# Kernel tuning notes

Hardware: AMD Instinct MI355X
Metric: run time of the kernel (lower is better)

Reference implementation:

```python
import jax, jax.numpy as jnp
import numpy as np
from jax import lax

EPS_LN = 1e-5
EPS_NORM = 1e-12
NUM_HEADS = 8
KV_HEADS = 2
REP = NUM_HEADS // KV_HEADS


def _layernorm_c(x, w, b):
    # WithBias LayerNorm over channel dim; x: [b,c,h,w]
    mu = x.mean(axis=1, keepdims=True)
    var = ((x - mu) ** 2).mean(axis=1, keepdims=True)
    return (x - mu) / jnp.sqrt(var + EPS_LN) * w[None, :, None, None] + b[None, :, None, None]


def _conv1x1(x, w):
    # x: [b,c,h,w], w: [o,c]
    return jnp.einsum('bchw,oc->bohw', x, w)


def _dwconv3x3(x, w):
    # depthwise 3x3, SAME padding; w: [C,1,3,3]
    C = x.shape[1]
    return lax.conv_general_dilated(
        x, w, window_strides=(1, 1), padding='SAME',
        dimension_numbers=('NCHW', 'OIHW', 'NCHW'), feature_group_count=C)


def _l2norm(x):
    # normalize over last axis (torch F.normalize semantics)
    n = jnp.sqrt(jnp.sum(x * x, axis=-1, keepdims=True))
    return x / jnp.maximum(n, EPS_NORM)


def setup_inputs() -> dict:
    key = jax.random.key(0)
    ks = jax.random.split(key, 8)
    b, dim, h, w = 4, 192, 256, 256
    kv_ch = 2 * dim // REP  # 96
    return {
        'x': jax.random.normal(ks[0], (b, dim, h, w), jnp.float32),
        'ln_w': jnp.ones((dim,), jnp.float32),
        'ln_b': jnp.zeros((dim,), jnp.float32),
        'q_w': jax.random.normal(ks[1], (dim, dim), jnp.float32) * 0.02,
        'q_dw': jax.random.normal(ks[2], (dim, 1, 3, 3), jnp.float32) * 0.1,
        'kv_w': jax.random.normal(ks[3], (kv_ch, dim), jnp.float32) * 0.02,
        'kv_dw': jax.random.normal(ks[4], (kv_ch, 1, 3, 3), jnp.float32) * 0.1,
        'proj_w': jax.random.normal(ks[5], (dim, dim), jnp.float32) * 0.02,
        'temperature': jnp.ones((NUM_HEADS, 1, 1), jnp.float32),
    }


def reference(x, ln_w, ln_b, q_w, q_dw, kv_w, kv_dw, proj_w, temperature):
    b, c, h, w = x.shape
    xn = _layernorm_c(x, ln_w, ln_b)
    q = _dwconv3x3(_conv1x1(xn, q_w), q_dw)            # [b, c, h, w]
    kv = _dwconv3x3(_conv1x1(xn, kv_w), kv_dw)         # [b, 2c/rep, h, w]
    k, v = jnp.split(kv, 2, axis=1)
    hw = h * w
    ch = c // NUM_HEADS
    q = q.reshape(b, NUM_HEADS, ch, hw)
    k = k.reshape(b, KV_HEADS, ch, hw)
    v = v.reshape(b, KV_HEADS, ch, hw)
    k = jnp.repeat(k, REP, axis=1)                     # repeat_kv
    v = jnp.repeat(v, REP, axis=1)
    q = _l2norm(q)
    k = _l2norm(k)
    attn = jnp.einsum('bhcn,bhdn->bhcd', q, k) * temperature[None]
    attn = jax.nn.softmax(attn, axis=-1)
    out = jnp.einsum('bhcd,bhdn->bhcn', attn, v)
    out = out.reshape(b, c, h, w)
    return _conv1x1(out, proj_w)
```

## Files before the change

### kernel.cpp

```cpp
#include <hip/hip_runtime.h>
#include <hip/hip_bf16.h>
#include <stdint.h>

#define HW    65536
#define NB    4
#define CIN   192
#define OYC   288
#define BSTR  200
#define EPS2  264

__device__ __forceinline__ float bflo(unsigned u){ return __uint_as_float(u << 16); }
__device__ __forceinline__ float bfhi(unsigned u){ return __uint_as_float(u & 0xffff0000u); }
__device__ __forceinline__ float bf2f(__hip_bfloat16 v){ return __bfloat162float(v); }
__device__ __forceinline__ unsigned short f2bfbits(float f){
  __hip_bfloat16 h = __float2bfloat16(f); return *(unsigned short*)&h;
}

__device__ __forceinline__ void unpack8(uint4 u, float* f) {
  f[0]=bflo(u.x); f[1]=bfhi(u.x); f[2]=bflo(u.y); f[3]=bfhi(u.y);
  f[4]=bflo(u.z); f[5]=bfhi(u.z); f[6]=bflo(u.w); f[7]=bfhi(u.w);
}

union BF8 { uint4 u; __hip_bfloat16 h[8]; };

typedef __attribute__((ext_vector_type(8))) short short8;
typedef __attribute__((ext_vector_type(4))) float floatx4;

__global__ void k_prep(const float* __restrict__ qw, const float* __restrict__ kvw,
                       const float* __restrict__ lnw, const float* __restrict__ lnb,
                       __hip_bfloat16* __restrict__ AF, float* __restrict__ bias,
                       float* __restrict__ Ssum) {
  int blk = blockIdx.x, t = threadIdx.x;
  if (blk < 32) {
    for (int i = blk * 256 + t; i < OYC * CIN; i += 32 * 256) {
      int o = i / CIN, c = i % CIN;
      float w = (o < 192) ? qw[o * 192 + c] : kvw[(o - 192) * 192 + c];
      float val = w * lnw[c];
      int ot = o >> 4, lo = o & 15;
      int ks = c >> 5, cr = c & 31, q = cr >> 3, j = cr & 7;
      int dst = (((ot * 6 + ks) * 64) + q * 16 + lo) * 8 + j;
      AF[dst] = __float2bfloat16(val);
    }
  } else {
    for (int o = t; o < OYC; o += 256) {
      float s = 0.f, s2 = 0.f;
      for (int c = 0; c < CIN; ++c) {
        float w = (o < 192) ? qw[o * 192 + c] : kvw[(o - 192) * 192 + c];
        s += w * lnb[c];
        s2 += bf2f(__float2bfloat16(w * lnw[c]));
      }
      bias[o] = s;
      Ssum[o] = s2;
    }
  }
}

__global__ __launch_bounds__(512, 2) void k_conv1r(const float* __restrict__ x,
                                                   const __hip_bfloat16* __restrict__ AF,
                                                   const float* __restrict__ bias,
                                                   const float* __restrict__ Ssum,
                                                   __hip_bfloat16* __restrict__ y) {
  __shared__ __align__(16) __hip_bfloat16 Bl[256 * BSTR];
  __shared__ float part_s[8][256];
  __shared__ float part_q[8][256];
  __shared__ float murs[256][2];
  __shared__ float biasl[OYC];
  __shared__ float Sl[OYC];

  int bid = blockIdx.x;
  int b = bid >> 8;
  int r = bid & 255;
  int tid = threadIdx.x;
  int w = tid >> 6, l = tid & 63;

  for (int i = tid; i < OYC; i += 512) { biasl[i] = bias[i]; Sl[i] = Ssum[i]; }

  {
    const float* xb = x + (size_t)(b * CIN + w * 24) * HW + r * 256 + l * 4;
    float s[4] = {0.f, 0.f, 0.f, 0.f}, q2[4] = {0.f, 0.f, 0.f, 0.f};
    unsigned pk[4][12];
#pragma unroll
    for (int c = 0; c < 24; ++c) {
      float4 v4 = *(const float4*)(xb + (size_t)c * HW);
      float vv[4] = {v4.x, v4.y, v4.z, v4.w};
#pragma unroll
      for (int i = 0; i < 4; ++i) {
        s[i] += vv[i]; q2[i] += vv[i] * vv[i];
        unsigned bits = f2bfbits(vv[i]);
        if ((c & 1) == 0) pk[i][c >> 1] = bits;
        else              pk[i][c >> 1] |= bits << 16;
      }
    }
#pragma unroll
    for (int i = 0; i < 4; ++i) {
      int px = l * 4 + i;
#pragma unroll
      for (int j = 0; j < 3; ++j) {
        uint4 u = make_uint4(pk[i][j*4], pk[i][j*4+1], pk[i][j*4+2], pk[i][j*4+3]);
        *(uint4*)&Bl[px * BSTR + w * 24 + j * 8] = u;
      }
    }
    *(float4*)&part_s[w][l * 4] = make_float4(s[0], s[1], s[2], s[3]);
    *(float4*)&part_q[w][l * 4] = make_float4(q2[0], q2[1], q2[2], q2[3]);
  }
  __syncthreads();

  int lane = tid & 63;
  int mh = w >> 2, nq = w & 3;
  int li = lane & 15, qd = lane >> 4;

  floatx4 acc[9][4];
#pragma unroll
  for (int t = 0; t < 9; ++t)
#pragma unroll
    for (int nt = 0; nt < 4; ++nt) acc[t][nt] = (floatx4){0.f, 0.f, 0.f, 0.f};

  const __hip_bfloat16* abase = AF + ((size_t)(mh * 9) * 6 * 64 + lane) * 8;
  short8 a0[9], a1[9];
#pragma unroll
  for (int t = 0; t < 9; ++t) a0[t] = *(const short8*)(abase + (size_t)(t * 6) * 512);

#pragma unroll
  for (int ks = 0; ks < 6; ++ks) {
    short8 bf[4];
#pragma unroll
    for (int nt = 0; nt < 4; ++nt) {
      int px = nq * 64 + nt * 16 + li;
      bf[nt] = *(const short8*)&Bl[px * BSTR + ks * 32 + qd * 8];
    }
    if (ks < 5) {
#pragma unroll
      for (int t = 0; t < 9; ++t) {
        short8 v = *(const short8*)(abase + (size_t)(t * 6 + ks + 1) * 512);
        if (ks & 1) a0[t] = v; else a1[t] = v;
      }
    }
#pragma unroll
    for (int t = 0; t < 9; ++t) {
      short8 af = (ks & 1) ? a1[t] : a0[t];
#pragma unroll
      for (int nt = 0; nt < 4; ++nt)
        acc[t][nt] = __builtin_amdgcn_mfma_f32_16x16x32_bf16(af, bf[nt], acc[t][nt], 0, 0, 0);
    }
  }

  if (tid < 256) {
    float s0 = 0.f, s1 = 0.f;
#pragma unroll
    for (int g = 0; g < 8; ++g) { s0 += part_s[g][tid]; s1 += part_q[g][tid]; }
    float m = s0 * (1.f / CIN);
    float var = s1 * (1.f / CIN) - m * m;
    murs[tid][0] = m;
    murs[tid][1] = rsqrtf(var + 1e-5f);
  }

  __hip_bfloat16* EP = Bl;
#pragma unroll
  for (int ph = 0; ph < 2; ++ph) {
    __syncthreads();
    if (mh == ph) {
#pragma unroll
      for (int t = 0; t < 9; ++t)
#pragma unroll
        for (int nt = 0; nt < 4; ++nt) {
          int px = nq * 64 + nt * 16 + li;
          float mu = murs[px][0], rs = murs[px][1];
#pragma unroll
          for (int rr = 0; rr < 4; ++rr) {
            int ol = t * 16 + qd * 4 + rr;
            float val = rs * (acc[t][nt][rr] - mu * Sl[ph * 144 + ol]) + biasl[ph * 144 + ol];
            EP[ol * EPS2 + px] = __float2bfloat16(val);
          }
        }
    }
    __syncthreads();
    for (int i = tid; i < 144 * 32; i += 512) {
      int row = i >> 5, seg = i & 31;
      uint4 u = *(const uint4*)&EP[row * EPS2 + seg * 8];
      *(uint4*)&y[(size_t)(b * OYC + ph * 144 + row) * HW + r * 256 + seg * 8] = u;
    }
  }
}

__global__ __launch_bounds__(256) void k_dwkv(const __hip_bfloat16* __restrict__ y,
                                              const float* __restrict__ kvdw,
                                              __hip_bfloat16* __restrict__ kbuf,
                                              __hip_bfloat16* __restrict__ vbuf,
                                              float* __restrict__ kss) {
  __shared__ __align__(16) __hip_bfloat16 stage[18 * 256];
  int bid = blockIdx.x;
  int hb = bid & 15;
  int ck = (bid >> 4) % 96;
  int b  = bid / (16 * 96);
  int tid = threadIdx.x;
  int h0 = hb * 16;

  const __hip_bfloat16* yp = y + (size_t)(b * OYC + 192 + ck) * HW;
  for (int i = tid; i < 18 * 32; i += 256) {
    int ry = i >> 5, seg = i & 31;
    int hh = h0 - 1 + ry;
    uint4 u = make_uint4(0u, 0u, 0u, 0u);
    if ((unsigned)hh < 256u) u = *(const uint4*)(yp + hh * 256 + seg * 8);
    *(uint4*)&stage[ry * 256 + seg * 8] = u;
  }
  __syncthreads();

  float w[9];
#pragma unroll
  for (int i = 0; i < 9; ++i) w[i] = kvdw[ck * 9 + i];

  int cg = tid & 31, rg = tid >> 5;
  int c0 = cg * 8;
  bool isk = (ck < 48);
  __hip_bfloat16* ob = (isk ? kbuf : vbuf) + (size_t)(b * 48 + (ck % 48)) * HW;
  float ssq = 0.f;
#pragma unroll
  for (int rr = 0; rr < 2; ++rr) {
    int orow = rg * 2 + rr;
    float o[8];
#pragma unroll
    for (int j = 0; j < 8; ++j) o[j] = 0.f;
#pragma unroll
    for (int ry = 0; ry < 3; ++ry) {
      const __hip_bfloat16* rb = &stage[(orow + ry) * 256];
      float v[8];
      unpack8(*(const uint4*)&rb[c0], v);
      float vl = (c0 > 0)       ? bf2f(rb[c0 - 1]) : 0.f;
      float vr = (c0 + 8 < 256) ? bf2f(rb[c0 + 8]) : 0.f;
      float wl = w[ry * 3], wm = w[ry * 3 + 1], wr = w[ry * 3 + 2];
      o[0] = fmaf(wl, vl, fmaf(wm, v[0], fmaf(wr, v[1], o[0])));
#pragma unroll
      for (int j = 1; j < 7; ++j)
        o[j] = fmaf(wl, v[j-1], fmaf(wm, v[j], fmaf(wr, v[j+1], o[j])));
      o[7] = fmaf(wl, v[6], fmaf(wm, v[7], fmaf(wr, vr, o[7])));
    }
    BF8 t;
#pragma unroll
    for (int j = 0; j < 8; ++j) {
      t.h[j] = __float2bfloat16(o[j]);
      if (isk) { float fv = bf2f(t.h[j]); ssq += fv * fv; }
    }
    *(uint4*)(ob + (size_t)(h0 + orow) * 256 + c0) = t.u;
  }
  if (isk) {
#pragma unroll
    for (int off = 32; off > 0; off >>= 1) ssq += __shfl_down(ssq, off);
    __shared__ float ws4[4];
    if ((tid & 63) == 0) ws4[tid >> 6] = ssq;
    __syncthreads();
    if (tid == 0) atomicAdd(&kss[b * 48 + ck], ws4[0] + ws4[1] + ws4[2] + ws4[3]);
  }
}

__global__ __launch_bounds__(512) void k_dwqk(const __hip_bfloat16* __restrict__ y,
                                              const float* __restrict__ qdw,
                                              const __hip_bfloat16* __restrict__ kbuf,
                                              float* __restrict__ qss,
                                              float* __restrict__ attn) {
  __shared__ __align__(16) __hip_bfloat16 ys[32 * 6 * 256];
  __shared__ __align__(16) __hip_bfloat16 ql[32 * 264];
  __shared__ __align__(16) __hip_bfloat16 kl[24 * 264];
  __shared__ float red[32 * 33];
  __shared__ float qssl[32];

  int t = blockIdx.x;
  int band = t & 63; t >>= 6;
  int qh = t % 3; t /= 3;
  int kvh = t & 1;
  int b = t >> 1;
  int tid = threadIdx.x;
  int r0 = band * 4;
  int chg0 = kvh * 96 + qh * 32;

  for (int i = tid; i < 32 * 33; i += 512) red[i] = 0.f;
  if (tid < 32) qssl[tid] = 0.f;

  for (int i = tid; i < 6144; i += 512) {
    int ch = i / 192, rem = i % 192;
    int ry = rem >> 5, seg = rem & 31;
    int hh = r0 - 1 + ry;
    uint4 u = make_uint4(0u, 0u, 0u, 0u);
    if ((unsigned)hh < 256u)
      u = *(const uint4*)(y + (size_t)(b * OYC + chg0 + ch) * HW + hh * 256 + seg * 8);
    *(uint4*)&ys[(ch * 6 + ry) * 256 + seg * 8] = u;
  }
  __syncthreads();

  int wv = tid >> 6, lane = tid & 63;
  int li = lane & 15, qd = lane >> 4;
  int kr1 = 16 + li; if (kr1 > 23) kr1 = 23;

  floatx4 acc[2][2];
  acc[0][0] = (floatx4){0.f,0.f,0.f,0.f}; acc[0][1] = (floatx4){0.f,0.f,0.f,0.f};
  acc[1][0] = (floatx4){0.f,0.f,0.f,0.f}; acc[1][1] = (floatx4){0.f,0.f,0.f,0.f};

  const __hip_bfloat16* kp = kbuf + (size_t)(b * 48 + kvh * 24) * HW;

  for (int rr = 0; rr < 4; ++rr) {
    if (rr) __syncthreads();
    for (int i = tid; i < 1024; i += 512) {
      int ch = i >> 5, seg = i & 31, c0 = seg * 8;
      const float* wp = qdw + (chg0 + ch) * 9;
      float o[8];
#pragma unroll
      for (int j = 0; j < 8; ++j) o[j] = 0.f;
#pragma unroll
      for (int ry = 0; ry < 3; ++ry) {
        const __hip_bfloat16* rb = &ys[(ch * 6 + rr + ry) * 256];
        float v[8];
        unpack8(*(const uint4*)&rb[c0], v);
        float vl = (c0 > 0)       ? bf2f(rb[c0 - 1]) : 0.f;
        float vr = (c0 + 8 < 256) ? bf2f(rb[c0 + 8]) : 0.f;
        float wl = wp[ry * 3], wm = wp[ry * 3 + 1], wr = wp[ry * 3 + 2];
        o[0] = fmaf(wl, vl, fmaf(wm, v[0], fmaf(wr, v[1], o[0])));
#pragma unroll
        for (int j = 1; j < 7; ++j)
          o[j] = fmaf(wl, v[j-1], fmaf(wm, v[j], fmaf(wr, v[j+1], o[j])));
        o[7] = fmaf(wl, v[6], fmaf(wm, v[7], fmaf(wr, vr, o[7])));
      }
      BF8 u; float part = 0.f;
#pragma unroll
      for (int j = 0; j < 8; ++j) {
        u.h[j] = __float2bfloat16(o[j]);
        float fv = bf2f(u.h[j]); part += fv * fv;
      }
      *(uint4*)&ql[ch * 264 + c0] = u.u;
      atomicAdd(&qssl[ch], part);
    }
    for (int i = tid; i < 768; i += 512) {
      int ch = i >> 5, seg = i & 31;
      *(uint4*)&kl[ch * 264 + seg * 8] =
        *(const uint4*)(kp + (size_t)ch * HW + (r0 + rr) * 256 + seg * 8);
    }
    __syncthreads();
    {
      int off = wv * 32 + qd * 8;
      short8 bk0 = *(const short8*)&kl[li  * 264 + off];
      short8 bk1 = *(const short8*)&kl[kr1 * 264 + off];
#pragma unroll
      for (int mt = 0; mt < 2; ++mt) {
        short8 aq = *(const short8*)&ql[(mt * 16 + li) * 264 + off];
        acc[mt][0] = __builtin_amdgcn_mfma_f32_16x16x32_bf16(aq, bk0, acc[mt][0], 0, 0, 0);
        acc[mt][1] = __builtin_amdgcn_mfma_f32_16x16x32_bf16(aq, bk1, acc[mt][1], 0, 0, 0);
      }
    }
  }
  __syncthreads();
#pragma unroll
  for (int mt = 0; mt < 2; ++mt) {
#pragma unroll
    for (int nt = 0; nt < 2; ++nt) {
      int n = nt * 16 + li;
      if (n < 24) {
#pragma unroll
        for (int r = 0; r < 4; ++r) {
          int m = mt * 16 + qd * 4 + r;
          atomicAdd(&red[m * 33 + n], acc[mt][nt][r]);
        }
      }
    }
  }
  __syncthreads();
  for (int i = tid; i < 32 * 24; i += 512) {
    int m = i / 24, d = i % 24;
    int cc = qh * 32 + m;
    int head = kvh * 4 + cc / 24, cp = cc % 24;
    atomicAdd(&attn[(((b * 8 + head) * 24) + cp) * 24 + d], red[m * 33 + d]);
  }
  if (tid < 32) atomicAdd(&qss[b * 192 + chg0 + tid], qssl[tid]);
}

__global__ void k_attn_final(const float* __restrict__ attn, const float* __restrict__ qss,
                             const float* __restrict__ kss, const float* __restrict__ temp,
                             const float* __restrict__ projw, __hip_bfloat16* __restrict__ AB) {
  int b = blockIdx.x;
  int t = threadIdx.x;
  __shared__ float as_[96 * 25];
  float acc[48];
#pragma unroll
  for (int j = 0; j < 48; ++j) acc[j] = 0.f;
  for (int kvh = 0; kvh < 2; ++kvh) {
    __syncthreads();
    if (t < 96) {
      int row = kvh * 96 + t;
      int h = row / 24, cp = row % 24;
      float rq = 1.f / fmaxf(sqrtf(qss[b * 192 + row]), 1e-12f);
      float tp = temp[h];
      float lg[24]; float mx = -1e30f;
#pragma unroll
      for (int d = 0; d < 24; ++d) {
        float rk = 1.f / fmaxf(sqrtf(kss[b * 48 + kvh * 24 + d]), 1e-12f);
        float l = attn[(((b * 8 + h) * 24) + cp) * 24 + d] * rq * rk * tp;
        lg[d] = l; mx = fmaxf(mx, l);
      }
      float s = 0.f;
#pragma unroll
      for (int d = 0; d < 24; ++d) { lg[d] = __expf(lg[d] - mx); s += lg[d]; }
      float inv = 1.f / s;
#pragma unroll
      for (int d = 0; d < 24; ++d) as_[t * 25 + d] = lg[d] * inv;
    }
    __syncthreads();
    if (t < 192) {
      for (int cc = 0; cc < 96; ++cc) {
        float pw = projw[t * 192 + kvh * 96 + cc];
        const float* ar = &as_[cc * 25];
#pragma unroll
        for (int d = 0; d < 24; ++d) acc[kvh * 24 + d] = fmaf(pw, ar[d], acc[kvh * 24 + d]);
      }
    }
  }
  if (t < 192) {
    __hip_bfloat16* ABb = AB + (size_t)b * 18432;
    int mt = t >> 4, lb = t & 15;
#pragma unroll
    for (int g = 0; g < 12; ++g) {
      int kk0 = g * 8;
      int s = kk0 >> 5;
      int lane = lb + 16 * ((kk0 & 31) >> 3);
      BF8 u;
#pragma unroll
      for (int jj = 0; jj < 8; ++jj) {
        int kk = kk0 + jj;
        if (kk < 48) {
          u.h[jj] = __float2bfloat16(acc[kk]);
        } else {
          int j = kk - 48;
          float hv = bf2f(__float2bfloat16(acc[j]));
          u.h[jj] = __float2bfloat16(acc[j] - hv);
        }
      }
      *(uint4*)(ABb + (size_t)((mt * 3 + s) * 64 + lane) * 8) = u.u;
    }
  }
}

__global__ __launch_bounds__(512) void k_out(const __hip_bfloat16* __restrict__ vbuf,
                                             const __hip_bfloat16* __restrict__ AB,
                                             float* __restrict__ out) {
  __shared__ __align__(16) __hip_bfloat16 vT[256 * 56];
  __shared__ __align__(16) float EPu[48 * 260];
  __hip_bfloat16* vl = (__hip_bfloat16*)EPu;

  int bid = blockIdx.x;
  int b  = bid >> 8;
  int n0 = (bid & 255) * 256;
  int tid = threadIdx.x;

  const __hip_bfloat16* vb = vbuf + (size_t)b * 48 * HW + n0;
  for (int i = tid; i < 48 * 32; i += 512) {
    int j = i >> 5, seg = i & 31;
    *(uint4*)&vl[j * 264 + seg * 8] = *(const uint4*)(vb + (size_t)j * HW + seg * 8);
  }
  __syncthreads();
  for (int i = tid; i < 256 * 6; i += 512) {
    int px = i & 255, j0 = (i >> 8) * 8;
    BF8 u;
#pragma unroll
    for (int e = 0; e < 8; ++e) u.h[e] = vl[(j0 + e) * 264 + px];
    *(uint4*)&vT[px * 56 + j0] = u.u;
  }
  __syncthreads();

  int w = tid >> 6, lane = tid & 63;
  int li = lane & 15, qd = lane >> 4;
  int mg = w & 3;
  int nh = w >> 2;

  const __hip_bfloat16* ABb = AB + (size_t)b * 18432;

  floatx4 acc[3][8];
#pragma unroll
  for (int m = 0; m < 3; ++m)
#pragma unroll
    for (int nt = 0; nt < 8; ++nt) acc[m][nt] = (floatx4){0.f, 0.f, 0.f, 0.f};

#pragma unroll
  for (int s = 0; s < 3; ++s) {
    short8 a[3];
#pragma unroll
    for (int m = 0; m < 3; ++m)
      a[m] = *(const short8*)(ABb + (size_t)(((mg * 3 + m) * 3 + s) * 64 + lane) * 8);
    int t0 = s * 32 + qd * 8;
    int j0 = (t0 >= 48) ? t0 - 48 : t0;
#pragma unroll
    for (int nt = 0; nt < 8; ++nt) {
      int n = nh * 128 + nt * 16 + li;
      short8 bv = *(const short8*)&vT[n * 56 + j0];
#pragma unroll
      for (int m = 0; m < 3; ++m)
        acc[m][nt] = __builtin_amdgcn_mfma_f32_16x16x32_bf16(a[m], bv, acc[m][nt], 0, 0, 0);
    }
  }

#pragma unroll
  for (int ph = 0; ph < 4; ++ph) {
    __syncthreads();
    if (mg == ph) {
#pragma unroll
      for (int m = 0; m < 3; ++m)
#pragma unroll
        for (int nt = 0; nt < 8; ++nt) {
          int col = nh * 128 + nt * 16 + li;
#pragma unroll
          for (int r = 0; r < 4; ++r)
            EPu[(m * 16 + qd * 4 + r) * 260 + col] = acc[m][nt][r];
        }
    }
    __syncthreads();
    for (int i = tid; i < 48 * 64; i += 512) {
      int row = i >> 6, c4 = (i & 63) * 4;
      float4 v4 = *(const float4*)&EPu[row * 260 + c4];
      *(float4*)&out[(size_t)(b * 192 + ph * 48 + row) * HW + n0 + c4] = v4;
    }
  }
}

extern "C" void kernel_launch(void* const* d_in, const int* in_sizes, int n_in,
                              void* d_out, int out_size, void* d_ws, size_t ws_size,
                              hipStream_t stream) {
  const float* x     = (const float*)d_in[0];
  const float* ln_w  = (const float*)d_in[1];
  const float* ln_b  = (const float*)d_in[2];
  const float* q_w   = (const float*)d_in[3];
  const float* q_dw  = (const float*)d_in[4];
  const float* kv_w  = (const float*)d_in[5];
  const float* kv_dw = (const float*)d_in[6];
  const float* projw = (const float*)d_in[7];
  const float* temp  = (const float*)d_in[8];
  float* out = (float*)d_out;
  float* wsf = (float*)d_ws;

  float* qss  = wsf;
  float* kss  = wsf + 768;
  float* attn = wsf + 960;
  __hip_bfloat16* AB = (__hip_bfloat16*)(wsf + 19392);
  float* bias = wsf + 56256;
  float* Ssum = wsf + 56544;
  __hip_bfloat16* AF = (__hip_bfloat16*)(wsf + 56832);
  __hip_bfloat16* y    = (__hip_bfloat16*)(wsf + 111872);
  __hip_bfloat16* kbuf = (__hip_bfloat16*)(wsf + 37860608);
  __hip_bfloat16* vbuf = (__hip_bfloat16*)(wsf + 44152064);

  hipMemsetAsync(wsf, 0, 19392 * sizeof(float), stream);
  hipLaunchKernelGGL(k_prep, dim3(33), dim3(256), 0, stream, q_w, kv_w, ln_w, ln_b, AF, bias, Ssum);
  hipLaunchKernelGGL(k_conv1r, dim3(NB * 256), dim3(512), 0, stream, x, AF, bias, Ssum, y);
  hipLaunchKernelGGL(k_dwkv, dim3(NB * 96 * 16), dim3(256), 0, stream, y, kv_dw, kbuf, vbuf, kss);
  hipLaunchKernelGGL(k_dwqk, dim3(NB * 2 * 3 * 64), dim3(512), 0, stream, y, q_dw, kbuf, qss, attn);
  hipLaunchKernelGGL(k_attn_final, dim3(NB), dim3(256), 0, stream, attn, qss, kss, temp, projw, AB);
  hipLaunchKernelGGL(k_out, dim3(NB * 256), dim3(512), 0, stream, vbuf, AB, out);
}
```

Baseline: 667.0 us.

## Double-buffer q/k tiles in dwqk and read y rows directly from global

Removes the large shared-memory staging of six y rows per channel and reads the depthwise-conv inputs straight from global memory. The q and k tiles are double-buffered so the next row's conv can overlap the current row's MFMA. Per-lane partial sums of squares are reduced with shuffles instead of a shared atomic per thread. Launch bounds request 4 blocks per CU. The lower LDS footprint should raise occupancy, at the cost of redundant global reads of neighbouring rows, which now depend on the cache.

Result: slower. 696.1 us (+4.4%).

```diff
diff --git a/kernel.cpp b/kernel.cpp
--- a/kernel.cpp
+++ b/kernel.cpp
@@ -252,14 +252,13 @@
   }
 }
 
-__global__ __launch_bounds__(512) void k_dwqk(const __hip_bfloat16* __restrict__ y,
-                                              const float* __restrict__ qdw,
-                                              const __hip_bfloat16* __restrict__ kbuf,
-                                              float* __restrict__ qss,
-                                              float* __restrict__ attn) {
-  __shared__ __align__(16) __hip_bfloat16 ys[32 * 6 * 256];
-  __shared__ __align__(16) __hip_bfloat16 ql[32 * 264];
-  __shared__ __align__(16) __hip_bfloat16 kl[24 * 264];
+__global__ __launch_bounds__(512, 4) void k_dwqk(const __hip_bfloat16* __restrict__ y,
+                                                 const float* __restrict__ qdw,
+                                                 const __hip_bfloat16* __restrict__ kbuf,
+                                                 float* __restrict__ qss,
+                                                 float* __restrict__ attn) {
+  __shared__ __align__(16) __hip_bfloat16 ql[2][32 * 264];
+  __shared__ __align__(16) __hip_bfloat16 kl[2][24 * 264];
   __shared__ float red[32 * 33];
   __shared__ float qssl[32];
 
@@ -275,40 +274,33 @@
   for (int i = tid; i < 32 * 33; i += 512) red[i] = 0.f;
   if (tid < 32) qssl[tid] = 0.f;
 
-  for (int i = tid; i < 6144; i += 512) {
-    int ch = i / 192, rem = i % 192;
-    int ry = rem >> 5, seg = rem & 31;
-    int hh = r0 - 1 + ry;
-    uint4 u = make_uint4(0u, 0u, 0u, 0u);
-    if ((unsigned)hh < 256u)
-      u = *(const uint4*)(y + (size_t)(b * OYC + chg0 + ch) * HW + hh * 256 + seg * 8);
-    *(uint4*)&ys[(ch * 6 + ry) * 256 + seg * 8] = u;
-  }
-  __syncthreads();
+  const __hip_bfloat16* yq = y + (size_t)(b * OYC + chg0) * HW;
+  const __hip_bfloat16* kp = kbuf + (size_t)(b * 48 + kvh * 24) * HW;
 
   int wv = tid >> 6, lane = tid & 63;
   int li = lane & 15, qd = lane >> 4;
   int kr1 = 16 + li; if (kr1 > 23) kr1 = 23;
 
-  floatx4 acc[2][2];
-  acc[0][0] = (floatx4){0.f,0.f,0.f,0.f}; acc[0][1] = (floatx4){0.f,0.f,0.f,0.f};
-  acc[1][0] = (floatx4){0.f,0.f,0.f,0.f}; acc[1][1] = (floatx4){0.f,0.f,0.f,0.f};
-
-  const __hip_bfloat16* kp = kbuf + (size_t)(b * 48 + kvh * 24) * HW;
-
-  for (int rr = 0; rr < 4; ++rr) {
-    if (rr) __syncthreads();
-    for (int i = tid; i < 1024; i += 512) {
+  float ssq0 = 0.f, ssq1 = 0.f;
+
+  auto produce = [&](int rr, int p) {
+    int hr = r0 + rr;
+#pragma unroll
+    for (int u = 0; u < 2; ++u) {
+      int i = tid + u * 512;
       int ch = i >> 5, seg = i & 31, c0 = seg * 8;
+      const __hip_bfloat16* cb = yq + (size_t)ch * HW;
       const float* wp = qdw + (chg0 + ch) * 9;
       float o[8];
 #pragma unroll
       for (int j = 0; j < 8; ++j) o[j] = 0.f;
 #pragma unroll
       for (int ry = 0; ry < 3; ++ry) {
-        const __hip_bfloat16* rb = &ys[(ch * 6 + rr + ry) * 256];
+        int hh = hr - 1 + ry;
+        if ((unsigned)hh >= 256u) continue;
+        const __hip_bfloat16* rb = cb + (size_t)hh * 256;
         float v[8];
-        unpack8(*(const uint4*)&rb[c0], v);
+        unpack8(*(const uint4*)(rb + c0), v);
         float vl = (c0 > 0)       ? bf2f(rb[c0 - 1]) : 0.f;
         float vr = (c0 + 8 < 256) ? bf2f(rb[c0 + 8]) : 0.f;
         float wl = wp[ry * 3], wm = wp[ry * 3 + 1], wr = wp[ry * 3 + 2];
@@ -318,34 +310,55 @@
           o[j] = fmaf(wl, v[j-1], fmaf(wm, v[j], fmaf(wr, v[j+1], o[j])));
         o[7] = fmaf(wl, v[6], fmaf(wm, v[7], fmaf(wr, vr, o[7])));
       }
-      BF8 u; float part = 0.f;
+      BF8 uu; float part = 0.f;
 #pragma unroll
       for (int j = 0; j < 8; ++j) {
-        u.h[j] = __float2bfloat16(o[j]);
-        float fv = bf2f(u.h[j]); part += fv * fv;
-      }
-      *(uint4*)&ql[ch * 264 + c0] = u.u;
-      atomicAdd(&qssl[ch], part);
+        uu.h[j] = __float2bfloat16(o[j]);
+        float fv = bf2f(uu.h[j]); part += fv * fv;
+      }
+      *(uint4*)&ql[p][ch * 264 + c0] = uu.u;
+      if (u == 0) ssq0 += part; else ssq1 += part;
     }
     for (int i = tid; i < 768; i += 512) {
       int ch = i >> 5, seg = i & 31;
-      *(uint4*)&kl[ch * 264 + seg * 8] =
-        *(const uint4*)(kp + (size_t)ch * HW + (r0 + rr) * 256 + seg * 8);
-    }
-    __syncthreads();
-    {
-      int off = wv * 32 + qd * 8;
-      short8 bk0 = *(const short8*)&kl[li  * 264 + off];
-      short8 bk1 = *(const short8*)&kl[kr1 * 264 + off];
-#pragma unroll
-      for (int mt = 0; mt < 2; ++mt) {
-        short8 aq = *(const short8*)&ql[(mt * 16 + li) * 264 + off];
-        acc[mt][0] = __builtin_amdgcn_mfma_f32_16x16x32_bf16(aq, bk0, acc[mt][0], 0, 0, 0);
-        acc[mt][1] = __builtin_amdgcn_mfma_f32_16x16x32_bf16(aq, bk1, acc[mt][1], 0, 0, 0);
-      }
-    }
-  }
+      *(uint4*)&kl[p][ch * 264 + seg * 8] =
+        *(const uint4*)(kp + (size_t)ch * HW + hr * 256 + seg * 8);
+    }
+  };
+
+  floatx4 acc[2][2];
+  acc[0][0] = (floatx4){0.f,0.f,0.f,0.f}; acc[0][1] = (floatx4){0.f,0.f,0.f,0.f};
+  acc[1][0] = (floatx4){0.f,0.f,0.f,0.f}; acc[1][1] = (floatx4){0.f,0.f,0.f,0.f};
+
+  produce(0, 0);
   __syncthreads();
+
+  for (int rr = 0; rr < 4; ++rr) {
+    int p = rr & 1;
+    if (rr < 3) produce(rr + 1, p ^ 1);
+    int off = wv * 32 + qd * 8;
+    short8 bk0 = *(const short8*)&kl[p][li  * 264 + off];
+    short8 bk1 = *(const short8*)&kl[p][kr1 * 264 + off];
+#pragma unroll
+    for (int mt = 0; mt < 2; ++mt) {
+      short8 aq = *(const short8*)&ql[p][(mt * 16 + li) * 264 + off];
+      acc[mt][0] = __builtin_amdgcn_mfma_f32_16x16x32_bf16(aq, bk0, acc[mt][0], 0, 0, 0);
+      acc[mt][1] = __builtin_amdgcn_mfma_f32_16x16x32_bf16(aq, bk1, acc[mt][1], 0, 0, 0);
+    }
+    __syncthreads();
+  }
+
+#pragma unroll
+  for (int off = 16; off > 0; off >>= 1) {
+    ssq0 += __shfl_down(ssq0, off, 32);
+    ssq1 += __shfl_down(ssq1, off, 32);
+  }
+  if ((lane & 31) == 0) {
+    int chA = tid >> 5;
+    atomicAdd(&qssl[chA], ssq0);
+    atomicAdd(&qssl[chA + 16], ssq1);
+  }
+
 #pragma unroll
   for (int mt = 0; mt < 2; ++mt) {
 #pragma unroll
```
